# Optimization experiments

Hardware: AMD Instinct MI355X
Metric: run time of the kernel (lower is better)

Reference implementation:

```python
import jax, jax.numpy as jnp
import numpy as np

N, H, W, C = 2, 96, 96, 256
HEADS, P = 8, 25
DH = C // HEADS
HID = int(C * 4.0)


def _ln(x, g, b):
    m = jnp.mean(x, axis=-1, keepdims=True)
    v = jnp.var(x, axis=-1, keepdims=True)
    return (x - m) / jnp.sqrt(v + 1e-5) * g + b


def _deform_sample(value, loc, h, w):
    # value: (n, heads, h*w, dh); loc: (n, Lq, heads, P, 2) normalized to [0,1] (x,y)
    # Bilinear sampling with align_corners=False and zero padding, as in
    # grid_sample used by MSDeformAttn.
    n = value.shape[0]
    gx = loc[..., 0] * w - 0.5
    gy = loc[..., 1] * h - 0.5
    x0 = jnp.floor(gx)
    y0 = jnp.floor(gy)
    fx = gx - x0
    fy = gy - y0
    out = jnp.zeros((n, HEADS, gx.shape[1] * P, DH), dtype=value.dtype)
    for dx, dy in ((0, 0), (1, 0), (0, 1), (1, 1)):
        xi = x0 + dx
        yi = y0 + dy
        wgt = (fx if dx else 1.0 - fx) * (fy if dy else 1.0 - fy)
        valid = ((xi >= 0) & (xi <= w - 1) & (yi >= 0) & (yi <= h - 1)).astype(value.dtype)
        xi_c = jnp.clip(xi, 0, w - 1).astype(jnp.int32)
        yi_c = jnp.clip(yi, 0, h - 1).astype(jnp.int32)
        idx = yi_c * w + xi_c                                   # (n, Lq, heads, P)
        idx = jnp.transpose(idx, (0, 2, 1, 3)).reshape(n, HEADS, -1)
        g = jnp.take_along_axis(value, idx[..., None], axis=2)  # (n, heads, Lq*P, dh)
        wv = jnp.transpose(wgt * valid, (0, 2, 1, 3)).reshape(n, HEADS, -1, 1)
        out = out + g * wv
    return out


def setup_inputs() -> dict:
    key = jax.random.key(0)
    ks = jax.random.split(key, 20)
    s = 0.02
    inp = {
        'x': jax.random.normal(ks[0], (N, H, W, C), jnp.float32),
        'ref_points': jax.random.uniform(ks[1], (N, H * W, 1, 2), jnp.float32),
        'spatial_shapes': jnp.array([[H, W]], dtype=jnp.int32),
        'level_start_index': jnp.zeros((1,), dtype=jnp.int32),
        'ln1_g': jnp.ones((C,), jnp.float32),
        'ln1_b': jnp.zeros((C,), jnp.float32),
        'w_off': jax.random.normal(ks[2], (C, HEADS * P * 2), jnp.float32) * s,
        'b_off': jax.random.normal(ks[3], (HEADS * P * 2,), jnp.float32) * s,
        'w_attn': jax.random.normal(ks[4], (C, HEADS * P), jnp.float32) * s,
        'b_attn': jax.random.normal(ks[5], (HEADS * P,), jnp.float32) * s,
        'w_val': jax.random.normal(ks[6], (C, C), jnp.float32) * s,
        'b_val': jnp.zeros((C,), jnp.float32),
        'w_out': jax.random.normal(ks[7], (C, C), jnp.float32) * s,
        'b_out': jnp.zeros((C,), jnp.float32),
        'ln2_g': jnp.ones((C,), jnp.float32),
        'ln2_b': jnp.zeros((C,), jnp.float32),
        'w_fc1': jax.random.normal(ks[8], (C, HID), jnp.float32) * s,
        'b_fc1': jnp.zeros((HID,), jnp.float32),
        'w_fc2': jax.random.normal(ks[9], (HID, C), jnp.float32) * s,
        'b_fc2': jnp.zeros((C,), jnp.float32),
    }
    return inp


def reference(x, ref_points, spatial_shapes, level_start_index,
              ln1_g, ln1_b, w_off, b_off, w_attn, b_attn,
              w_val, b_val, w_out, b_out, ln2_g, ln2_b,
              w_fc1, b_fc1, w_fc2, b_fc2):
    n, h, w, c = x.shape
    lq = h * w
    shortcut = x
    # pre-norm + flatten to query
    q = _ln(x, ln1_g, ln1_b).reshape(n, lq, c)
    # MSDeformAttn (n_levels = 1)
    value = (q @ w_val + b_val).reshape(n, lq, HEADS, DH).transpose(0, 2, 1, 3)
    off = (q @ w_off + b_off).reshape(n, lq, HEADS, P, 2)
    aw = jax.nn.softmax((q @ w_attn + b_attn).reshape(n, lq, HEADS, P), axis=-1)
    norm = jnp.array([w, h], dtype=x.dtype)          # offsets normalized by (W, H)
    ref = ref_points[:, :, 0, :]                     # (n, Lq, 2)
    loc = ref[:, :, None, None, :] + off / norm      # (n, Lq, heads, P, 2)
    sampled = _deform_sample(value, loc, h, w).reshape(n, HEADS, lq, P, DH)
    attn = jnp.einsum('nqhp,nhqpd->nqhd', aw, sampled).reshape(n, lq, c)
    attn = attn @ w_out + b_out
    x1 = shortcut + attn.reshape(n, h, w, c)
    # MLP block
    y = _ln(x1, ln2_g, ln2_b)
    y = jax.nn.gelu(y @ w_fc1 + b_fc1, approximate=False) @ w_fc2 + b_fc2
    return x1 + y
```

## Files before the change

### kernel.cpp

```cpp
#include <hip/hip_runtime.h>
#include <hip/hip_bf16.h>
#include <math.h>

typedef __hip_bfloat16 bf16;
typedef __attribute__((ext_vector_type(8))) short short8;
typedef __attribute__((ext_vector_type(4))) float f32x4;

#define NB 2
#define HH 96
#define WW 96
#define CC 256
#define NHEADS 8
#define PP 25
#define DHH 32
#define HIDN 1024
#define LQ (HH*WW)
#define TT (NB*LQ)
#define NVC 896
#define TB 8

__device__ __forceinline__ float b2f(bf16 v){ return __bfloat162float(v); }
__device__ __forceinline__ bf16  f2b(float v){ return __float2bfloat16(v); }
__device__ __forceinline__ float lo_bf(unsigned u){ return __uint_as_float(u << 16); }
__device__ __forceinline__ float hi_bf(unsigned u){ return __uint_as_float(u & 0xffff0000u); }

__device__ __forceinline__ void gl2lds16(const void* g, void* l) {
    __builtin_amdgcn_global_load_lds(
        (const __attribute__((address_space(1))) unsigned int*)g,
        (__attribute__((address_space(3))) unsigned int*)l, 16, 0, 0);
}

__global__ __launch_bounds__(256) void prep_all(const float* __restrict__ w_val,
                                                const float* __restrict__ w_off,
                                                const float* __restrict__ w_attn,
                                                const float* __restrict__ w_fc1,
                                                const float* __restrict__ w_fc2,
                                                const float* __restrict__ w_out,
                                                const float* __restrict__ b_val,
                                                const float* __restrict__ b_off,
                                                const float* __restrict__ b_attn,
                                                bf16* __restrict__ wvcT,
                                                bf16* __restrict__ wfc1T,
                                                bf16* __restrict__ wfc2T,
                                                bf16* __restrict__ woutT,
                                                float* __restrict__ bvc)
{
    const int idx = blockIdx.x*256 + threadIdx.x;
    if (idx < 229376) {
        int n = idx >> 8, k = idx & 255;
        float v = (n < 256) ? w_val[(size_t)k*256 + n]
                : (n < 656) ? w_off[(size_t)k*400 + (n-256)]
                : (n < 856) ? w_attn[(size_t)k*200 + (n-656)] : 0.f;
        wvcT[idx] = f2b(v);
    } else if (idx < 491520) {
        int j = idx - 229376; int n = j >> 8, k = j & 255;
        wfc1T[j] = f2b(w_fc1[(size_t)k*1024 + n]);
    } else if (idx < 753664) {
        int j = idx - 491520; int n = j >> 10, k = j & 1023;
        wfc2T[j] = f2b(w_fc2[(size_t)k*256 + n]);
    } else if (idx < 819200) {
        int j = idx - 753664; int n = j >> 8, k = j & 255;
        woutT[j] = f2b(w_out[(size_t)k*256 + n]);
    }
    if (idx < NVC)
        bvc[idx] = (idx < 256) ? b_val[idx]
                 : (idx < 656) ? b_off[idx-256]
                 : (idx < 856) ? b_attn[idx-656] : 0.f;
}

__global__ __launch_bounds__(256) void ln_kernel(const float* __restrict__ x,
                                                 const float* __restrict__ g,
                                                 const float* __restrict__ b,
                                                 bf16* __restrict__ out)
{
    const int t = blockIdx.x*4 + (threadIdx.x >> 6);
    const int l = threadIdx.x & 63;
    const float4 v = *(const float4*)(x + (size_t)t*CC + l*4);
    float s  = v.x + v.y + v.z + v.w;
    float s2 = v.x*v.x + v.y*v.y + v.z*v.z + v.w*v.w;
    #pragma unroll
    for (int m = 1; m < 64; m <<= 1) { s += __shfl_xor(s, m); s2 += __shfl_xor(s2, m); }
    const float mean = s * (1.f/CC);
    const float var  = s2 * (1.f/CC) - mean*mean;
    const float rs   = 1.f / sqrtf(var + 1e-5f);
    const float4 gg = *(const float4*)(g + l*4);
    const float4 bb = *(const float4*)(b + l*4);
    bf16 o[4];
    o[0] = f2b((v.x-mean)*rs*gg.x + bb.x);
    o[1] = f2b((v.y-mean)*rs*gg.y + bb.y);
    o[2] = f2b((v.z-mean)*rs*gg.z + bb.z);
    o[3] = f2b((v.w-mean)*rs*gg.w + bb.w);
    *(uint2*)(out + (size_t)t*CC + l*4) = *(uint2*)o;
}

template<int EPI, int K, int N, int TM>
__global__ __launch_bounds__(256) void mfma_gemm(const bf16* __restrict__ A,
                                                 const bf16* __restrict__ Bt,
                                                 const float* __restrict__ bias,
                                                 void* __restrict__ outv,
                                                 const float* __restrict__ resid,
                                                 float* __restrict__ val32)
{
    constexpr int AR  = TM/8;
    constexpr int TR  = AR + 16;
    constexpr int RPW = TR/4;
    constexpr int NJ  = (TM==128) ? 4 : 2;
    __shared__ short As[TM*64];
    __shared__ short Bs[128*64];
    const int tid = threadIdx.x;
    const int w = tid >> 6, l = tid & 63;
    const int bm = blockIdx.x, bn = blockIdx.y;

    const bf16* sbase[RPW];
    short*      lbase[RPW];
    {
        const int lrow = l >> 3;
        const int q    = (l & 7) ^ lrow;
        #pragma unroll
        for (int j = 0; j < RPW; j++) {
            int r = w*RPW + j;
            bool isA = r < AR;
            int rr = isA ? r : r - AR;
            int row = rr*8 + lrow;
            size_t grow = (size_t)(isA ? (bm*TM + row) : (bn*128 + row));
            sbase[j] = (isA ? A : Bt) + grow*K + q*8;
            lbase[j] = (isA ? As : Bs) + rr*512;
        }
    }

    const int mbase = (TM==128) ? 64*(w >> 1) : 0;
    const int nbase = (TM==128) ? 64*(w & 1)  : 32*w;

    int aoff[2][4], boff[2][NJ];
    #pragma unroll
    for (int s = 0; s < 2; s++) {
        const int q = s*4 + (l >> 4);
        #pragma unroll
        for (int i = 0; i < 4; i++) {
            int m = mbase + i*16 + (l & 15);
            aoff[s][i] = (m*8 + (q ^ (m & 7))) * 8;
        }
        #pragma unroll
        for (int j = 0; j < NJ; j++) {
            int n = nbase + j*16 + (l & 15);
            boff[s][j] = (n*8 + (q ^ (n & 7))) * 8;
        }
    }

    f32x4 acc[4][NJ];
    #pragma unroll
    for (int i = 0; i < 4; i++)
        #pragma unroll
        for (int j = 0; j < NJ; j++)
            acc[i][j] = (f32x4){0.f, 0.f, 0.f, 0.f};

    for (int k0 = 0; k0 < K; k0 += 64) {
        #pragma unroll
        for (int j = 0; j < RPW; j++)
            gl2lds16(sbase[j] + k0, lbase[j]);
        __syncthreads();
        #pragma unroll
        for (int s = 0; s < 2; s++) {
            short8 af[4], bfr[NJ];
            #pragma unroll
            for (int i = 0; i < 4; i++)  af[i]  = *(const short8*)(As + aoff[s][i]);
            #pragma unroll
            for (int j = 0; j < NJ; j++) bfr[j] = *(const short8*)(Bs + boff[s][j]);
            #pragma unroll
            for (int i = 0; i < 4; i++)
                #pragma unroll
                for (int j = 0; j < NJ; j++)
                    acc[i][j] = __builtin_amdgcn_mfma_f32_16x16x32_bf16(af[i], bfr[j], acc[i][j], 0, 0, 0);
        }
        __syncthreads();
    }

    const int row0 = bm*TM + mbase + (l >> 4)*4;
    const int col0 = bn*128 + nbase + (l & 15);
    #pragma unroll
    for (int i = 0; i < 4; i++) {
        #pragma unroll
        for (int j = 0; j < NJ; j++) {
            const int col = col0 + j*16;
            const float bs = bias[col];
            #pragma unroll
            for (int r = 0; r < 4; r++) {
                const int row = row0 + i*16 + r;
                float v = acc[i][j][r] + bs;
                size_t o = (size_t)row * N + col;
                if (EPI == 0) {
                    ((bf16*)outv)[o] = f2b(v);
                } else if (EPI == 2) {
                    ((bf16*)outv)[o] = f2b(0.5f * v * (1.f + erff(v * 0.70710678118654752f)));
                } else if (EPI == 3) {
                    ((float*)outv)[o] = v + resid[o];
                } else {
                    if (col < 256) val32[(size_t)row*CC + col] = v;
                    else           ((bf16*)outv)[o] = f2b(v);
                }
            }
        }
    }
}

struct __align__(16) Tap { _Float16 w[4]; unsigned short i[4]; };

__global__ __launch_bounds__(256) void sample_kernel(const bf16* __restrict__ vc,
                                                     const float* __restrict__ val32,
                                                     const float* __restrict__ refp,
                                                     bf16* __restrict__ samp)
{
    __shared__ Tap taps[TB*200];
    const int b = blockIdx.x;
    const int tbase = ((b & 7)*288 + (b >> 3)) * TB;
    const int tid = threadIdx.x;

    {
        const int pair = tid >> 2;
        const int j    = tid & 3;
        const int tl   = pair >> 3;
        const int h    = pair & 7;
        const int t    = tbase + tl;
        const bf16* row = vc + (size_t)t*NVC;

        float lg[7];
        #pragma unroll
        for (int k = 0; k < 7; k++) {
            int p = j + 4*k;
            lg[k] = (p < PP) ? b2f(row[656 + h*25 + p]) : -1e30f;
        }
        float m = lg[0];
        #pragma unroll
        for (int k = 1; k < 7; k++) m = fmaxf(m, lg[k]);
        m = fmaxf(m, __shfl_xor(m, 1));
        m = fmaxf(m, __shfl_xor(m, 2));
        float s = 0.f;
        float ex[7];
        #pragma unroll
        for (int k = 0; k < 7; k++) {
            ex[k] = (j + 4*k < PP) ? expf(lg[k] - m) : 0.f;
            s += ex[k];
        }
        s += __shfl_xor(s, 1);
        s += __shfl_xor(s, 2);
        const float inv = 1.f / s;

        const float rx96 = refp[(size_t)t*2 + 0]*96.f - 0.5f;
        const float ry96 = refp[(size_t)t*2 + 1]*96.f - 0.5f;
        const unsigned* offp = (const unsigned*)(row + 256 + h*50);

        #pragma unroll
        for (int k = 0; k < 7; k++) {
            const int p = j + 4*k;
            if (p >= PP) break;
            const float a = ex[k] * inv;
            const unsigned uo = offp[p];
            const float gx = rx96 + lo_bf(uo);
            const float gy = ry96 + hi_bf(uo);
            const float x0f = floorf(gx), y0f = floorf(gy);
            const float fx = gx - x0f, fy = gy - y0f;
            const int ix = (int)x0f, iy = (int)y0f;
            Tap tp;
            #pragma unroll
            for (int d = 0; d < 4; d++) {
                const int dx = d & 1, dy = d >> 1;
                const int xi = ix + dx, yi = iy + dy;
                const bool valid = (xi >= 0) & (xi <= WW-1) & (yi >= 0) & (yi <= HH-1);
                const int xc = min(max(xi, 0), WW-1);
                const int yc = min(max(yi, 0), HH-1);
                tp.i[d] = (unsigned short)(yc*WW + xc);
                tp.w[d] = (_Float16)(valid ? a * (dx ? fx : 1.f-fx) * (dy ? fy : 1.f-fy) : 0.f);
            }
            taps[tl*200 + h*25 + p] = tp;
        }
    }
    __syncthreads();

    const int wv_ = tid >> 6, l = tid & 63;
    const int tl  = wv_*2 + (l >> 5);
    const int r   = l & 31;
    const int h   = r >> 2, oct = r & 3;
    const int c0  = h*DHH + oct*8;
    const int t   = tbase + tl;
    const int n   = (t >= LQ) ? 1 : 0;
    const float* pv = val32 + (size_t)n*LQ*CC + c0;
    const int pib = tl*200 + h*25;

    float acc[8] = {0.f,0.f,0.f,0.f,0.f,0.f,0.f,0.f};
    for (int p = 0; p < PP; p++) {
        const uint4 tv = *((const uint4*)taps + (pib + p));
        const _Float16* wp_ = (const _Float16*)&tv;
        const unsigned short* ip_ = (const unsigned short*)&tv + 4;
        #pragma unroll
        for (int d = 0; d < 4; d++) {
            const float wt = (float)wp_[d];
            const float* vp = pv + (size_t)ip_[d]*CC;
            const float4 v0 = *(const float4*)(vp);
            const float4 v1 = *(const float4*)(vp + 4);
            acc[0] += wt*v0.x; acc[1] += wt*v0.y;
            acc[2] += wt*v0.z; acc[3] += wt*v0.w;
            acc[4] += wt*v1.x; acc[5] += wt*v1.y;
            acc[6] += wt*v1.z; acc[7] += wt*v1.w;
        }
    }
    bf16 o[8];
    #pragma unroll
    for (int j2 = 0; j2 < 8; j2++) o[j2] = f2b(acc[j2]);
    *(uint4*)(samp + (size_t)t*CC + c0) = *(uint4*)o;
}

extern "C" void kernel_launch(void* const* d_in, const int* in_sizes, int n_in,
                              void* d_out, int out_size, void* d_ws, size_t ws_size,
                              hipStream_t stream)
{
    const float* x      = (const float*)d_in[0];
    const float* refp   = (const float*)d_in[1];
    const float* ln1_g  = (const float*)d_in[4];
    const float* ln1_b  = (const float*)d_in[5];
    const float* w_off  = (const float*)d_in[6];
    const float* b_off  = (const float*)d_in[7];
    const float* w_attn = (const float*)d_in[8];
    const float* b_attn = (const float*)d_in[9];
    const float* w_val  = (const float*)d_in[10];
    const float* b_val  = (const float*)d_in[11];
    const float* w_out  = (const float*)d_in[12];
    const float* b_out  = (const float*)d_in[13];
    const float* ln2_g  = (const float*)d_in[14];
    const float* ln2_b  = (const float*)d_in[15];
    const float* w_fc1  = (const float*)d_in[16];
    const float* b_fc1  = (const float*)d_in[17];
    const float* w_fc2  = (const float*)d_in[18];
    const float* b_fc2  = (const float*)d_in[19];

    char* wsb = (char*)d_ws;
    bf16*  q     = (bf16*)(wsb + 0);
    bf16*  vc    = (bf16*)(wsb + 9437184);
    bf16*  samp  = (bf16*)(wsb + 42467328);
    float* x1    = (float*)(wsb + 51904512);
    bf16*  wvcT  = (bf16*)(wsb + 70778880);
    bf16*  wfc1T = (bf16*)(wsb + 71237632);
    bf16*  wfc2T = (bf16*)(wsb + 71761920);
    bf16*  woutT = (bf16*)(wsb + 72286208);
    float* bvc   = (float*)(wsb + 72417280);
    float* val32 = (float*)(wsb + 72420864);
    bf16*  hid   = (bf16*)(wsb + 0);
    bf16*  y0    = samp;

    if (ws_size < 91295232) return;

    const dim3 blk(256);
    prep_all<<<dim3(3200), blk, 0, stream>>>(w_val, w_off, w_attn, w_fc1, w_fc2, w_out,
                                             b_val, b_off, b_attn,
                                             wvcT, wfc1T, wfc2T, woutT, bvc);
    ln_kernel<<<dim3(TT/4), blk, 0, stream>>>(x, ln1_g, ln1_b, q);
    mfma_gemm<4,256,NVC,128><<<dim3(TT/128, NVC/128), blk, 0, stream>>>(q, wvcT, bvc, (void*)vc, nullptr, val32);
    sample_kernel<<<dim3(TT/TB), blk, 0, stream>>>(vc, val32, refp, samp);
    mfma_gemm<3,256,CC,64><<<dim3(TT/64, CC/128), blk, 0, stream>>>(samp, woutT, b_out, (void*)x1, x, nullptr);
    ln_kernel<<<dim3(TT/4), blk, 0, stream>>>(x1, ln2_g, ln2_b, y0);
    mfma_gemm<2,256,HIDN,128><<<dim3(TT/128, HIDN/128), blk, 0, stream>>>(y0, wfc1T, b_fc1, (void*)hid, nullptr, nullptr);
    mfma_gemm<3,HIDN,CC,64><<<dim3(TT/64, CC/128), blk, 0, stream>>>(hid, wfc2T, b_fc2, d_out, x1, nullptr);
}
```

Measured before the change: 275.8 us.

## Store value tensor as head-major bf16 to shrink deformable-sampling gathers

The value projection is now written as bf16 in a (batch, head, position, dh) layout instead of fp32 row-major, so each gathered tap reads a contiguous 16-byte chunk from a 64-byte head row. This halves gather bytes and improves cache-line locality in the bilinear sampling loop, which is likely bandwidth bound on random reads. The sampling loop is also partially unrolled. Values lose precision relative to fp32, and the GEMM epilogue now does scattered 2-byte stores.

Measured after the change: 276.3 us. About the same (+0.2%).

```diff
diff --git a/kernel.cpp b/kernel.cpp
--- a/kernel.cpp
+++ b/kernel.cpp
@@ -99,7 +99,7 @@
                                                  const float* __restrict__ bias,
                                                  void* __restrict__ outv,
                                                  const float* __restrict__ resid,
-                                                 float* __restrict__ val32)
+                                                 bf16* __restrict__ val_t)
 {
     constexpr int AR  = TM/8;
     constexpr int TR  = AR + 16;
@@ -195,8 +195,14 @@
                 } else if (EPI == 3) {
                     ((float*)outv)[o] = v + resid[o];
                 } else {
-                    if (col < 256) val32[(size_t)row*CC + col] = v;
-                    else           ((bf16*)outv)[o] = f2b(v);
+                    if (col < 256) {
+                        const int n_  = (row >= LQ) ? 1 : 0;
+                        const int lq_ = row - n_*LQ;
+                        const int h_  = col >> 5, dh_ = col & 31;
+                        val_t[((size_t)(n_*NHEADS + h_)*LQ + lq_)*DHH + dh_] = f2b(v);
+                    } else {
+                        ((bf16*)outv)[o] = f2b(v);
+                    }
                 }
             }
         }
@@ -206,7 +212,7 @@
 struct __align__(16) Tap { _Float16 w[4]; unsigned short i[4]; };
 
 __global__ __launch_bounds__(256) void sample_kernel(const bf16* __restrict__ vc,
-                                                     const float* __restrict__ val32,
+                                                     const bf16* __restrict__ val_t,
                                                      const float* __restrict__ refp,
                                                      bf16* __restrict__ samp)
 {
@@ -283,10 +289,11 @@
     const int c0  = h*DHH + oct*8;
     const int t   = tbase + tl;
     const int n   = (t >= LQ) ? 1 : 0;
-    const float* pv = val32 + (size_t)n*LQ*CC + c0;
+    const bf16* pv = val_t + (size_t)(n*NHEADS + h)*LQ*DHH + oct*8;
     const int pib = tl*200 + h*25;
 
     float acc[8] = {0.f,0.f,0.f,0.f,0.f,0.f,0.f,0.f};
+    #pragma unroll 5
     for (int p = 0; p < PP; p++) {
         const uint4 tv = *((const uint4*)taps + (pib + p));
         const _Float16* wp_ = (const _Float16*)&tv;
@@ -294,13 +301,11 @@
         #pragma unroll
         for (int d = 0; d < 4; d++) {
             const float wt = (float)wp_[d];
-            const float* vp = pv + (size_t)ip_[d]*CC;
-            const float4 v0 = *(const float4*)(vp);
-            const float4 v1 = *(const float4*)(vp + 4);
-            acc[0] += wt*v0.x; acc[1] += wt*v0.y;
-            acc[2] += wt*v0.z; acc[3] += wt*v0.w;
-            acc[4] += wt*v1.x; acc[5] += wt*v1.y;
-            acc[6] += wt*v1.z; acc[7] += wt*v1.w;
+            const uint4 vv = *(const uint4*)(pv + (size_t)ip_[d]*DHH);
+            acc[0] += wt*lo_bf(vv.x); acc[1] += wt*hi_bf(vv.x);
+            acc[2] += wt*lo_bf(vv.y); acc[3] += wt*hi_bf(vv.y);
+            acc[4] += wt*lo_bf(vv.z); acc[5] += wt*hi_bf(vv.z);
+            acc[6] += wt*lo_bf(vv.w); acc[7] += wt*hi_bf(vv.w);
         }
     }
     bf16 o[8];
@@ -342,19 +347,19 @@
     bf16*  wfc2T = (bf16*)(wsb + 71761920);
     bf16*  woutT = (bf16*)(wsb + 72286208);
     float* bvc   = (float*)(wsb + 72417280);
-    float* val32 = (float*)(wsb + 72420864);
+    bf16*  val_t = (bf16*)(wsb + 72420864);
     bf16*  hid   = (bf16*)(wsb + 0);
     bf16*  y0    = samp;
 
-    if (ws_size < 91295232) return;
+    if (ws_size < 81858048) return;
 
     const dim3 blk(256);
     prep_all<<<dim3(3200), blk, 0, stream>>>(w_val, w_off, w_attn, w_fc1, w_fc2, w_out,
                                              b_val, b_off, b_attn,
                                              wvcT, wfc1T, wfc2T, woutT, bvc);
     ln_kernel<<<dim3(TT/4), blk, 0, stream>>>(x, ln1_g, ln1_b, q);
-    mfma_gemm<4,256,NVC,128><<<dim3(TT/128, NVC/128), blk, 0, stream>>>(q, wvcT, bvc, (void*)vc, nullptr, val32);
-    sample_kernel<<<dim3(TT/TB), blk, 0, stream>>>(vc, val32, refp, samp);
+    mfma_gemm<4,256,NVC,128><<<dim3(TT/128, NVC/128), blk, 0, stream>>>(q, wvcT, bvc, (void*)vc, nullptr, val_t);
+    sample_kernel<<<dim3(TT/TB), blk, 0, stream>>>(vc, val_t, refp, samp);
     mfma_gemm<3,256,CC,64><<<dim3(TT/64, CC/128), blk, 0, stream>>>(samp, woutT, b_out, (void*)x1, x, nullptr);
     ln_kernel<<<dim3(TT/4), blk, 0, stream>>>(x1, ln2_g, ln2_b, y0);
     mfma_gemm<2,256,HIDN,128><<<dim3(TT/128, HIDN/128), blk, 0, stream>>>(y0, wfc1T, b_fc1, (void*)hid, nullptr, nullptr);
```
